# Kernel optimization log

Hardware: AMD Instinct MI355X
Metric: run time of the kernel (lower is better)

Reference implementation:

```python
import jax, jax.numpy as jnp
import numpy as np

N_NODES = 100000
N_GRAPHS = 64


def _gcn_norm(edge_index, num_nodes):
    # Add self-loops and compute symmetric normalization (PyG GCNConv gcn_norm).
    src = jnp.concatenate([edge_index[0], jnp.arange(num_nodes, dtype=edge_index.dtype)])
    dst = jnp.concatenate([edge_index[1], jnp.arange(num_nodes, dtype=edge_index.dtype)])
    deg = jax.ops.segment_sum(jnp.ones_like(dst, dtype=jnp.float32), dst, num_segments=num_nodes)
    dinv = jnp.where(deg > 0, jax.lax.rsqrt(deg), 0.0)
    norm = dinv[src] * dinv[dst]  # [E + N]
    return src, dst, norm


def _gcn_conv(x, src, dst, norm, W, b, num_nodes):
    h = x @ W                                   # [N, out]
    msg = h[src] * norm[:, None]                # gather + scale  [E+N, out]
    out = jax.ops.segment_sum(msg, dst, num_segments=num_nodes)  # scatter-add
    return out + b


def setup_inputs() -> dict:
    key = jax.random.key(0)
    ks = jax.random.split(key, 8)
    E = 1600000
    pos = jax.random.normal(ks[0], (N_NODES, 3), dtype=jnp.float32)
    edge_index = jax.random.randint(ks[1], (2, E), 0, N_NODES, dtype=jnp.int64)
    batch = jnp.sort(jax.random.randint(ks[2], (N_NODES,), 0, N_GRAPHS, dtype=jnp.int64))
    def glorot(k, shape):
        lim = np.sqrt(6.0 / (shape[0] + shape[1])).astype(np.float32)
        return jax.random.uniform(k, shape, dtype=jnp.float32, minval=-lim, maxval=lim)
    return {
        "pos": pos,
        "edge_index": edge_index,
        "batch": batch,
        "W1": glorot(ks[3], (3, 64)),  "b1": jnp.zeros((64,), jnp.float32),
        "W2": glorot(ks[4], (64, 64)), "b2": jnp.zeros((64,), jnp.float32),
        "W3": glorot(ks[5], (64, 24)), "b3": jnp.zeros((24,), jnp.float32),
    }


def reference(pos, edge_index, batch, W1, b1, W2, b2, W3, b3):
    src, dst, norm = _gcn_norm(edge_index, N_NODES)
    h = jax.nn.relu(_gcn_conv(pos, src, dst, norm, W1, b1, N_NODES))
    h = jax.nn.relu(_gcn_conv(h, src, dst, norm, W2, b2, N_NODES))
    y = _gcn_conv(h, src, dst, norm, W3, b3, N_NODES)  # [N, 24]
    # global_mean_pool over batch ids, then tanh
    sums = jax.ops.segment_sum(y, batch, num_segments=N_GRAPHS)          # [G, 24]
    counts = jax.ops.segment_sum(jnp.ones((N_NODES,), jnp.float32), batch, num_segments=N_GRAPHS)
    mean = sums / jnp.maximum(counts, 1.0)[:, None]
    return jnp.tanh(mean)
```

## Files before the change

### kernel.cpp

```cpp
#include <hip/hip_runtime.h>
#include <math.h>

#define NNODES 100000
#define NGRAPHS 64
#define NB 391
#define CAP 4608
#define NBLKA 1024
#define NBLKB 512
#define NT2 1563


__device__ __forceinline__ unsigned int f2bf(float x) {
    union { float f; unsigned int u; } v;
    v.f = x;
    unsigned int r = v.u + 0x7FFFu + ((v.u >> 16) & 1u);
    return r >> 16;
}
__device__ __forceinline__ unsigned int pack2bf(float lo, float hi) {
    return f2bf(lo) | (f2bf(hi) << 16);
}
__device__ __forceinline__ float bflo(unsigned int u) {
    union { unsigned int u; float f; } v;
    v.u = u << 16;
    return v.f;
}
__device__ __forceinline__ float bfhi(unsigned int u) {
    union { unsigned int u; float f; } v;
    v.u = u & 0xFFFF0000u;
    return v.f;
}

#define ACC8(A, ofs, V) \
    A[(ofs) + 0] += bflo((V).x); A[(ofs) + 1] += bfhi((V).x); \
    A[(ofs) + 2] += bflo((V).y); A[(ofs) + 3] += bfhi((V).y); \
    A[(ofs) + 4] += bflo((V).z); A[(ofs) + 5] += bfhi((V).z); \
    A[(ofs) + 6] += bflo((V).w); A[(ofs) + 7] += bfhi((V).w);


__device__ __forceinline__ int ntld(const int* p) { return __builtin_nontemporal_load(p); }
__device__ __forceinline__ int2 ntld2(const int2* p) {
    long long v = __builtin_nontemporal_load((const long long*)p);
    int2 r;
    r.x = (int)(unsigned int)(v & 0xffffffffLL);
    r.y = (int)(v >> 32);
    return r;
}


__global__ void bucket_scatter(const int* __restrict__ src, const int* __restrict__ dst,
                               int* __restrict__ bCur, unsigned int* __restrict__ packed,
                               int E) {
    __shared__ int h[NB];
    __shared__ int cur[NB];
    for (int k = threadIdx.x; k < NB; k += 256) h[k] = 0;
    __syncthreads();
    int base = blockIdx.x * 2048 + threadIdx.x;
    int d[8], s[8], b[8];
#pragma unroll
    for (int k = 0; k < 8; ++k) {
        int e = base + k * 256;
        if (e < E) {
            d[k] = dst[e];
            s[k] = src[e];
            b[k] = d[k] >> 8;
            atomicAdd(&h[b[k]], 1);
        }
    }
    __syncthreads();
    for (int k = threadIdx.x; k < NB; k += 256) {
        int c = h[k];
        cur[k] = c ? atomicAdd(&bCur[k], c) : 0;
    }
    __syncthreads();
#pragma unroll
    for (int k = 0; k < 8; ++k) {
        int e = base + k * 256;
        if (e < E) {
            int pos = atomicAdd(&cur[b[k]], 1);
            if (pos < CAP)
                packed[(size_t)b[k] * CAP + pos] = ((unsigned int)(d[k] & 255) << 17) | (unsigned int)s[k];
        }
    }
}

__global__ void bucket_build(const unsigned int* __restrict__ packed, const int* __restrict__ bCur,
                             const int* __restrict__ batch, const float* __restrict__ pos,
                             int2* __restrict__ rowBE, int* __restrict__ col,
                             float* __restrict__ dinv, int2* __restrict__ dg,
                             float4* __restrict__ pos4, int N_) {
    __shared__ int cnt[256];
    __shared__ int bas[256];
    int tid = threadIdx.x;
    int b = blockIdx.x;
    int count = bCur[b];
    if (count > CAP) count = CAP;
    int beg = b * CAP;
    cnt[tid] = 0;
    __syncthreads();
    for (int k = beg + tid; k < beg + count; k += 256) atomicAdd(&cnt[packed[k] >> 17], 1);
    __syncthreads();
    int myCnt = cnt[tid];
    bas[tid] = myCnt;
    __syncthreads();
    for (int off = 1; off < 256; off <<= 1) {
        int v = (tid >= off) ? bas[tid - off] : 0;
        __syncthreads();
        bas[tid] += v;
        __syncthreads();
    }
    int excl = beg + ((tid > 0) ? bas[tid - 1] : 0);
    int node = (b << 8) + tid;
    if (node < N_) {
        rowBE[node] = make_int2(excl, excl + myCnt);
        float di = rsqrtf((float)myCnt + 1.0f);
        dinv[node] = di;
        dg[node] = make_int2(__float_as_int(di), batch[node]);
        pos4[node] = make_float4(pos[node * 3] * di, pos[node * 3 + 1] * di,
                                 pos[node * 3 + 2] * di, di);
    }
    __syncthreads();
    bas[tid] = excl;
    __syncthreads();
    for (int k = beg + tid; k < beg + count; k += 256) {
        unsigned int p = packed[k];
        int pos_ = atomicAdd(&bas[p >> 17], 1);
        col[pos_] = (int)(p & 0x1FFFFu);
    }
}


__global__ void mm12_gp(const float4* __restrict__ pos4, const int2* __restrict__ rowBE,
                        const int* __restrict__ col, const float* __restrict__ dinv,
                        const float* __restrict__ W1, const float* __restrict__ b1,
                        const float* __restrict__ W2, uint2* __restrict__ outz, int n) {
    __shared__ float4 part[256];
    __shared__ float4 ag[64];
    __shared__ float xs[64][65];
    __shared__ float4 ws[64 * 16];
    const int tid = threadIdx.x;
    const int rowBase = blockIdx.x * 64;
    const int r = tid >> 2, t4 = tid & 3;
    const int i = rowBase + r;

    float sx = 0, sy = 0, sz = 0, dival = 0;
    if (i < n) {
        int2 be = rowBE[i];
        float4 ps = pos4[i];
        dival = ps.w;
        if (t4 == 0) { sx = ps.x; sy = ps.y; sz = ps.z; }
        for (int j = be.x + t4; j < be.y; j += 4) {
            float4 v = pos4[ntld(&col[j])];
            sx += v.x; sy += v.y; sz += v.z;
        }
    }
    part[tid] = make_float4(sx, sy, sz, dival);
    const float4* W24 = (const float4*)W2;
    for (int idx = tid; idx < 64 * 16; idx += 256) ws[idx] = W24[idx];
    __syncthreads();
    if (tid < 64) {
        float4 p0 = part[tid * 4], p1 = part[tid * 4 + 1];
        float4 p2 = part[tid * 4 + 2], p3 = part[tid * 4 + 3];
        ag[tid] = make_float4((p0.x + p1.x) + (p2.x + p3.x),
                              (p0.y + p1.y) + (p2.y + p3.y),
                              (p0.z + p1.z) + (p2.z + p3.z), p0.w);
    }
    __syncthreads();
    for (int idx = tid; idx < 64 * 64; idx += 256) {
        int rr = idx >> 6;
        int k = idx & 63;
        float4 a = ag[rr];
        float v = b1[k] + a.w * (a.x * W1[k] + a.y * W1[64 + k] + a.z * W1[128 + k]);
        xs[rr][k] = fmaxf(v, 0.0f);
    }
    __syncthreads();

    const int f4 = tid & 15;
    const int r0 = (tid >> 4) * 4;
    float4 a0 = make_float4(0, 0, 0, 0), a1 = a0, a2 = a0, a3 = a0;
#pragma unroll 4
    for (int k = 0; k < 64; ++k) {
        float4 wv = ws[k * 16 + f4];
        float xa = xs[r0 + 0][k];
        float xb = xs[r0 + 1][k];
        float xc = xs[r0 + 2][k];
        float xd = xs[r0 + 3][k];
        a0.x += wv.x * xa; a0.y += wv.y * xa; a0.z += wv.z * xa; a0.w += wv.w * xa;
        a1.x += wv.x * xb; a1.y += wv.y * xb; a1.z += wv.z * xb; a1.w += wv.w * xb;
        a2.x += wv.x * xc; a2.y += wv.y * xc; a2.z += wv.z * xc; a2.w += wv.w * xc;
        a3.x += wv.x * xd; a3.y += wv.y * xd; a3.z += wv.z * xd; a3.w += wv.w * xd;
    }
    int i0 = rowBase + r0;
    float d0 = (i0 + 0 < n) ? dinv[i0 + 0] : 1.0f;
    float d1 = (i0 + 1 < n) ? dinv[i0 + 1] : 1.0f;
    float d2 = (i0 + 2 < n) ? dinv[i0 + 2] : 1.0f;
    float d3 = (i0 + 3 < n) ? dinv[i0 + 3] : 1.0f;
    const size_t gsel = (size_t)(f4 >> 2) * NNODES;
    const int sub = f4 & 3;
    if (i0 + 0 < n)
        outz[(gsel + (i0 + 0)) * 4 + sub] = make_uint2(pack2bf(a0.x * d0, a0.y * d0), pack2bf(a0.z * d0, a0.w * d0));
    if (i0 + 1 < n)
        outz[(gsel + (i0 + 1)) * 4 + sub] = make_uint2(pack2bf(a1.x * d1, a1.y * d1), pack2bf(a1.z * d1, a1.w * d1));
    if (i0 + 2 < n)
        outz[(gsel + (i0 + 2)) * 4 + sub] = make_uint2(pack2bf(a2.x * d2, a2.y * d2), pack2bf(a2.z * d2, a2.w * d2));
    if (i0 + 3 < n)
        outz[(gsel + (i0 + 3)) * 4 + sub] = make_uint2(pack2bf(a3.x * d3, a3.y * d3), pack2bf(a3.z * d3, a3.w * d3));
}


__global__ void gather2_sliced(const int2* __restrict__ rowBE, const int* __restrict__ col,
                               const uint4* __restrict__ z2s, const float* __restrict__ dinv,
                               const float* __restrict__ b2, uint4* __restrict__ h2s) {
    const int tid = threadIdx.x;
    const int g = blockIdx.x / NT2;
    const int tile = blockIdx.x - g * NT2;
    const int il = tid >> 2, t4 = tid & 3;
    const int i = tile * 64 + il;
    const size_t base = (size_t)g * NNODES;

    float acc[16];
#pragma unroll
    for (int k = 0; k < 16; ++k) acc[k] = 0.0f;

    if (i < NNODES) {
        if (t4 == 0) {
            uint4 sa = z2s[(base + i) * 2 + 0];
            uint4 sb = z2s[(base + i) * 2 + 1];
            ACC8(acc, 0, sa)
            ACC8(acc, 8, sb)
        }
        int2 be = rowBE[i];
        int j = be.x + t4;
        for (; j + 4 < be.y; j += 8) {
            int s0 = ntld(&col[j]);
            int s1 = ntld(&col[j + 4]);
            uint4 a0 = z2s[(base + s0) * 2 + 0];
            uint4 b0 = z2s[(base + s0) * 2 + 1];
            uint4 a1 = z2s[(base + s1) * 2 + 0];
            uint4 b1 = z2s[(base + s1) * 2 + 1];
            ACC8(acc, 0, a0)
            ACC8(acc, 8, b0)
            ACC8(acc, 0, a1)
            ACC8(acc, 8, b1)
        }
        for (; j < be.y; j += 4) {
            int s = ntld(&col[j]);
            uint4 a = z2s[(base + s) * 2 + 0];
            uint4 b = z2s[(base + s) * 2 + 1];
            ACC8(acc, 0, a)
            ACC8(acc, 8, b)
        }
    }
#pragma unroll
    for (int k = 0; k < 16; ++k) acc[k] += __shfl_xor(acc[k], 1);
#pragma unroll
    for (int k = 0; k < 16; ++k) acc[k] += __shfl_xor(acc[k], 2);

    if (t4 == 0 && i < NNODES) {
        float di = dinv[i];
        const float* bv = b2 + g * 16;
        float h[16];
#pragma unroll
        for (int k = 0; k < 16; ++k) h[k] = fmaxf(acc[k] * di + bv[k], 0.0f);
        h2s[(base + i) * 2 + 0] = make_uint4(pack2bf(h[0], h[1]), pack2bf(h[2], h[3]),
                                             pack2bf(h[4], h[5]), pack2bf(h[6], h[7]));
        h2s[(base + i) * 2 + 1] = make_uint4(pack2bf(h[8], h[9]), pack2bf(h[10], h[11]),
                                             pack2bf(h[12], h[13]), pack2bf(h[14], h[15]));
    }
}


__device__ __forceinline__ void st_y(uint2* __restrict__ yA, uint2* __restrict__ yB,
                                     int i, int f4, uint2 v) {
    if (f4 < 4) yA[(size_t)i * 4 + f4] = v;
    else        yB[(size_t)i * 2 + (f4 - 4)] = v;
}

__global__ void mm3_b16(const uint4* __restrict__ xb, const float* __restrict__ W,
                        const float* __restrict__ dinv, uint2* __restrict__ yA,
                        uint2* __restrict__ yB, int n) {
    __shared__ float xs[128][65];
    __shared__ float4 ws[64 * 6];
    const int tid = threadIdx.x;
    const int rowBase = blockIdx.x * 128;

    for (int idx = tid; idx < 128 * 8; idx += 192) {
        int r = idx >> 3;
        int c8 = idx & 7;
        int gr = rowBase + r;
        uint4 v = (gr < n) ? xb[((size_t)(c8 >> 1) * NNODES + gr) * 2 + (c8 & 1)]
                           : make_uint4(0, 0, 0, 0);
        float* xp = &xs[r][c8 * 8];
        xp[0] = bflo(v.x); xp[1] = bfhi(v.x);
        xp[2] = bflo(v.y); xp[3] = bfhi(v.y);
        xp[4] = bflo(v.z); xp[5] = bfhi(v.z);
        xp[6] = bflo(v.w); xp[7] = bfhi(v.w);
    }
    const float4* W4 = (const float4*)W;
    for (int idx = tid; idx < 64 * 6; idx += 192) ws[idx] = W4[idx];
    __syncthreads();

    const int f4 = tid % 6;
    const int r0 = (tid / 6) * 4;
    float4 a0 = make_float4(0, 0, 0, 0), a1 = a0, a2 = a0, a3 = a0;
#pragma unroll 4
    for (int k = 0; k < 64; ++k) {
        float4 wv = ws[k * 6 + f4];
        float xa = xs[r0 + 0][k];
        float xb_ = xs[r0 + 1][k];
        float xc = xs[r0 + 2][k];
        float xd = xs[r0 + 3][k];
        a0.x += wv.x * xa; a0.y += wv.y * xa; a0.z += wv.z * xa; a0.w += wv.w * xa;
        a1.x += wv.x * xb_; a1.y += wv.y * xb_; a1.z += wv.z * xb_; a1.w += wv.w * xb_;
        a2.x += wv.x * xc; a2.y += wv.y * xc; a2.z += wv.z * xc; a2.w += wv.w * xc;
        a3.x += wv.x * xd; a3.y += wv.y * xd; a3.z += wv.z * xd; a3.w += wv.w * xd;
    }
    int i0 = rowBase + r0;
    float d0 = (i0 + 0 < n) ? dinv[i0 + 0] : 1.0f;
    float d1 = (i0 + 1 < n) ? dinv[i0 + 1] : 1.0f;
    float d2 = (i0 + 2 < n) ? dinv[i0 + 2] : 1.0f;
    float d3 = (i0 + 3 < n) ? dinv[i0 + 3] : 1.0f;
    if (i0 + 0 < n)
        st_y(yA, yB, i0 + 0, f4, make_uint2(pack2bf(a0.x * d0, a0.y * d0), pack2bf(a0.z * d0, a0.w * d0)));
    if (i0 + 1 < n)
        st_y(yA, yB, i0 + 1, f4, make_uint2(pack2bf(a1.x * d1, a1.y * d1), pack2bf(a1.z * d1, a1.w * d1)));
    if (i0 + 2 < n)
        st_y(yA, yB, i0 + 2, f4, make_uint2(pack2bf(a2.x * d2, a2.y * d2), pack2bf(a2.z * d2, a2.w * d2)));
    if (i0 + 3 < n)
        st_y(yA, yB, i0 + 3, f4, make_uint2(pack2bf(a3.x * d3, a3.y * d3), pack2bf(a3.z * d3, a3.w * d3)));
}


__global__ void gather3A(const int2* __restrict__ rowBE, const int* __restrict__ col,
                         const uint4* __restrict__ yA, const int2* __restrict__ dg,
                         float* __restrict__ partA) {
    __shared__ float lpool[NGRAPHS * 16];
    for (int k = threadIdx.x; k < NGRAPHS * 16; k += 256) lpool[k] = 0.0f;
    __syncthreads();

    const int T = NNODES * 4;
    const int stride = NBLKA * 256;
    for (int t = blockIdx.x * 256 + threadIdx.x; t < T; t += stride) {
        int i = t >> 2;
        int half = t & 1;
        int r = (t >> 1) & 1;
        int2 wi = ntld2(&dg[i]);
        float di = __int_as_float(wi.x);
        int g = wi.y;
        int2 be = ntld2(&rowBE[i]);
        int mid = be.x + ((be.y - be.x + 1) >> 1);
        int a = half ? mid : be.x;
        int b = half ? be.y : mid;
        float acc[8] = {0, 0, 0, 0, 0, 0, 0, 0};
        if (!half) {
            uint4 sv = yA[(size_t)i * 2 + r];
            acc[0] = bflo(sv.x); acc[1] = bfhi(sv.x);
            acc[2] = bflo(sv.y); acc[3] = bfhi(sv.y);
            acc[4] = bflo(sv.z); acc[5] = bfhi(sv.z);
            acc[6] = bflo(sv.w); acc[7] = bfhi(sv.w);
        }
        int j = a;
        for (; j + 8 <= b; j += 8) {
            int s[8];
            uint4 v[8];
#pragma unroll
            for (int k = 0; k < 8; ++k) s[k] = ntld(&col[j + k]);
#pragma unroll
            for (int k = 0; k < 8; ++k) v[k] = yA[(size_t)s[k] * 2 + r];
#pragma unroll
            for (int k = 0; k < 8; ++k) {
                acc[0] += bflo(v[k].x); acc[1] += bfhi(v[k].x);
                acc[2] += bflo(v[k].y); acc[3] += bfhi(v[k].y);
                acc[4] += bflo(v[k].z); acc[5] += bfhi(v[k].z);
                acc[6] += bflo(v[k].w); acc[7] += bfhi(v[k].w);
            }
        }
        for (; j < b; ++j) {
            uint4 v = yA[(size_t)ntld(&col[j]) * 2 + r];
            acc[0] += bflo(v.x); acc[1] += bfhi(v.x);
            acc[2] += bflo(v.y); acc[3] += bfhi(v.y);
            acc[4] += bflo(v.z); acc[5] += bfhi(v.z);
            acc[6] += bflo(v.w); acc[7] += bfhi(v.w);
        }
#pragma unroll
        for (int k = 0; k < 8; ++k) acc[k] += __shfl_xor(acc[k], 1);
        if (!half) {
            float* lp = &lpool[g * 16 + r * 8];
#pragma unroll
            for (int k = 0; k < 8; ++k) atomicAdd(&lp[k], acc[k] * di);
        }
    }
    __syncthreads();
    float* pp = partA + (size_t)blockIdx.x * (NGRAPHS * 16);
    for (int k = threadIdx.x; k < NGRAPHS * 16; k += 256) pp[k] = lpool[k];
}

__global__ void gather3B(const int2* __restrict__ rowBE, const int* __restrict__ col,
                         const uint4* __restrict__ yB, const int2* __restrict__ dg,
                         float* __restrict__ partB, float* __restrict__ cpart) {
    __shared__ float lpool[NGRAPHS * 8];
    __shared__ float lcnt[NGRAPHS];
    for (int k = threadIdx.x; k < NGRAPHS * 8; k += 256) lpool[k] = 0.0f;
    for (int k = threadIdx.x; k < NGRAPHS; k += 256) lcnt[k] = 0.0f;
    __syncthreads();

    const int T = NNODES * 2;
    const int stride = NBLKB * 256;
    for (int t = blockIdx.x * 256 + threadIdx.x; t < T; t += stride) {
        int i = t >> 1;
        int half = t & 1;
        int2 wi = ntld2(&dg[i]);
        float di = __int_as_float(wi.x);
        int g = wi.y;
        int2 be = ntld2(&rowBE[i]);
        int mid = be.x + ((be.y - be.x + 1) >> 1);
        int a = half ? mid : be.x;
        int b = half ? be.y : mid;
        float acc[8] = {0, 0, 0, 0, 0, 0, 0, 0};
        if (!half) {
            uint4 sv = yB[i];
            acc[0] = bflo(sv.x); acc[1] = bfhi(sv.x);
            acc[2] = bflo(sv.y); acc[3] = bfhi(sv.y);
            acc[4] = bflo(sv.z); acc[5] = bfhi(sv.z);
            acc[6] = bflo(sv.w); acc[7] = bfhi(sv.w);
        }
        int j = a;
        for (; j + 8 <= b; j += 8) {
            int s[8];
            uint4 v[8];
#pragma unroll
            for (int k = 0; k < 8; ++k) s[k] = ntld(&col[j + k]);
#pragma unroll
            for (int k = 0; k < 8; ++k) v[k] = yB[s[k]];
#pragma unroll
            for (int k = 0; k < 8; ++k) {
                acc[0] += bflo(v[k].x); acc[1] += bfhi(v[k].x);
                acc[2] += bflo(v[k].y); acc[3] += bfhi(v[k].y);
                acc[4] += bflo(v[k].z); acc[5] += bfhi(v[k].z);
                acc[6] += bflo(v[k].w); acc[7] += bfhi(v[k].w);
            }
        }
        for (; j < b; ++j) {
            uint4 v = yB[ntld(&col[j])];
            acc[0] += bflo(v.x); acc[1] += bfhi(v.x);
            acc[2] += bflo(v.y); acc[3] += bfhi(v.y);
            acc[4] += bflo(v.z); acc[5] += bfhi(v.z);
            acc[6] += bflo(v.w); acc[7] += bfhi(v.w);
        }
#pragma unroll
        for (int k = 0; k < 8; ++k) acc[k] += __shfl_xor(acc[k], 1);
        if (!half) {
            float* lp = &lpool[g * 8];
#pragma unroll
            for (int k = 0; k < 8; ++k) atomicAdd(&lp[k], acc[k] * di);
            atomicAdd(&lcnt[g], 1.0f);
        }
    }
    __syncthreads();
    float* pp = partB + (size_t)blockIdx.x * (NGRAPHS * 8);
    for (int k = threadIdx.x; k < NGRAPHS * 8; k += 256) pp[k] = lpool[k];
    float* cp = cpart + (size_t)blockIdx.x * NGRAPHS;
    for (int k = threadIdx.x; k < NGRAPHS; k += 256) cp[k] = lcnt[k];
}

__global__ void pool_finish(const float* __restrict__ partA, const float* __restrict__ partB,
                            const float* __restrict__ cpart, const float* __restrict__ b3,
                            float* __restrict__ out) {
    int w = blockIdx.x * 4 + (threadIdx.x >> 6);
    int lane = threadIdx.x & 63;
    if (w >= NGRAPHS * 24) return;
    int g = w / 24;
    int c = w - g * 24;
    float s = 0.0f, cn = 0.0f;
    if (c < 16) {
        for (int b = lane; b < NBLKA; b += 64) s += partA[(size_t)b * (NGRAPHS * 16) + g * 16 + c];
    } else {
        for (int b = lane; b < NBLKB; b += 64) s += partB[(size_t)b * (NGRAPHS * 8) + g * 8 + (c - 16)];
    }
    for (int b = lane; b < NBLKB; b += 64) cn += cpart[(size_t)b * NGRAPHS + g];
#pragma unroll
    for (int off = 32; off > 0; off >>= 1) {
        s += __shfl_down(s, off);
        cn += __shfl_down(cn, off);
    }
    if (lane == 0) out[w] = tanhf(s / fmaxf(cn, 1.0f) + b3[c]);
}


static inline int gridFor(long long total, int block) {
    return (int)((total + block - 1) / block);
}

extern "C" void kernel_launch(void* const* d_in, const int* in_sizes, int n_in,
                              void* d_out, int out_size, void* d_ws, size_t ws_size,
                              hipStream_t stream) {
    const float* pos   = (const float*)d_in[0];
    const int*   ei    = (const int*)d_in[1];
    const int*   batch = (const int*)d_in[2];
    const float* W1    = (const float*)d_in[3];
    const float* b1    = (const float*)d_in[4];
    const float* W2    = (const float*)d_in[5];
    const float* b2    = (const float*)d_in[6];
    const float* W3    = (const float*)d_in[7];
    const float* b3    = (const float*)d_in[8];
    float*       out   = (float*)d_out;

    const int N = NNODES;
    const int E = in_sizes[1] / 2;
    const int* src = ei;
    const int* dst = ei + E;

    char* p = (char*)d_ws;
    uint4*  z2s    = (uint4*)p;         p += (size_t)N * 8 * sizeof(uint4);
    uint4*  h2s    = (uint4*)p;         p += (size_t)N * 8 * sizeof(uint4);
    uint4*  yA     = (uint4*)p;         p += (size_t)N * 2 * sizeof(uint4);
    uint4*  yB     = (uint4*)p;         p += (size_t)N * 1 * sizeof(uint4);
    float4* pos4   = (float4*)p;        p += (size_t)N * sizeof(float4);
    int2*   rowBE  = (int2*)p;          p += (size_t)N * sizeof(int2);
    int2*   dg     = (int2*)p;          p += (size_t)N * sizeof(int2);
    float*  dinv   = (float*)p;         p += (size_t)N * sizeof(float);
    int*    bCur   = (int*)p;           p += NB * sizeof(int);
    unsigned int* packed = (unsigned int*)p;  p += (size_t)NB * CAP * sizeof(unsigned int);
    int*    col    = (int*)p;           p += (size_t)NB * CAP * sizeof(int);
    float*  partA  = (float*)z2s;
    float*  partB  = partA + (size_t)NBLKA * NGRAPHS * 16;
    float*  cpartB = partB + (size_t)NBLKB * NGRAPHS * 8;

    const int B = 256;
    const int edgeBlocks = gridFor(E, 2048);

    hipMemsetAsync(bCur, 0, NB * sizeof(int), stream);
    bucket_scatter<<<edgeBlocks, 256, 0, stream>>>(src, dst, bCur, packed, E);
    bucket_build<<<NB, 256, 0, stream>>>(packed, bCur, batch, pos, rowBE, col, dinv, dg, pos4, N);

    mm12_gp<<<gridFor(N, 64), 256, 0, stream>>>(pos4, rowBE, col, dinv, W1, b1, W2, (uint2*)z2s, N);

    gather2_sliced<<<4 * NT2, 256, 0, stream>>>(rowBE, col, z2s, dinv, b2, h2s);

    mm3_b16<<<gridFor(N, 128), 192, 0, stream>>>(h2s, W3, dinv, (uint2*)yA, (uint2*)yB, N);

    gather3A<<<NBLKA, 256, 0, stream>>>(rowBE, col, yA, dg, partA);
    gather3B<<<NBLKB, 256, 0, stream>>>(rowBE, col, yB, dg, partB, cpartB);
    pool_finish<<<gridFor((long long)NGRAPHS * 24 * 64, B), B, 0, stream>>>(partA, partB, cpartB, b3, out);
}
```

Baseline: 287.6 us.

## Split gather2 into per-slice launches with two threads per node

The layer-2 aggregation kernel now assigns two threads per node, each owning half of a 16-feature slice, instead of four threads striding the edge list and reducing with shuffles. The four feature slices are launched as four separate kernels rather than one grid indexed by slice. This removes the cross-lane shuffle reduction and gives each thread longer sequential edge loops with four independent gathers in flight. In exchange it adds three extra launches, and per-thread edge work grows for high-degree nodes.

```diff
diff --git a/kernel.cpp b/kernel.cpp
--- a/kernel.cpp
+++ b/kernel.cpp
@@ -7,7 +7,6 @@
 #define CAP 4608
 #define NBLKA 1024
 #define NBLKB 512
-#define NT2 1563
 
 
 __device__ __forceinline__ unsigned int f2bf(float x) {
@@ -209,63 +208,49 @@
 
 __global__ void gather2_sliced(const int2* __restrict__ rowBE, const int* __restrict__ col,
                                const uint4* __restrict__ z2s, const float* __restrict__ dinv,
-                               const float* __restrict__ b2, uint4* __restrict__ h2s) {
+                               const float* __restrict__ b2, uint4* __restrict__ h2s, int g) {
     const int tid = threadIdx.x;
-    const int g = blockIdx.x / NT2;
-    const int tile = blockIdx.x - g * NT2;
-    const int il = tid >> 2, t4 = tid & 3;
-    const int i = tile * 64 + il;
+    const int il = tid >> 1, t2 = tid & 1;
+    const int i = blockIdx.x * 128 + il;
+    if (i >= NNODES) return;
     const size_t base = (size_t)g * NNODES;
 
-    float acc[16];
-#pragma unroll
-    for (int k = 0; k < 16; ++k) acc[k] = 0.0f;
-
-    if (i < NNODES) {
-        if (t4 == 0) {
-            uint4 sa = z2s[(base + i) * 2 + 0];
-            uint4 sb = z2s[(base + i) * 2 + 1];
-            ACC8(acc, 0, sa)
-            ACC8(acc, 8, sb)
-        }
-        int2 be = rowBE[i];
-        int j = be.x + t4;
-        for (; j + 4 < be.y; j += 8) {
-            int s0 = ntld(&col[j]);
-            int s1 = ntld(&col[j + 4]);
-            uint4 a0 = z2s[(base + s0) * 2 + 0];
-            uint4 b0 = z2s[(base + s0) * 2 + 1];
-            uint4 a1 = z2s[(base + s1) * 2 + 0];
-            uint4 b1 = z2s[(base + s1) * 2 + 1];
-            ACC8(acc, 0, a0)
-            ACC8(acc, 8, b0)
-            ACC8(acc, 0, a1)
-            ACC8(acc, 8, b1)
-        }
-        for (; j < be.y; j += 4) {
-            int s = ntld(&col[j]);
-            uint4 a = z2s[(base + s) * 2 + 0];
-            uint4 b = z2s[(base + s) * 2 + 1];
-            ACC8(acc, 0, a)
-            ACC8(acc, 8, b)
-        }
-    }
-#pragma unroll
-    for (int k = 0; k < 16; ++k) acc[k] += __shfl_xor(acc[k], 1);
-#pragma unroll
-    for (int k = 0; k < 16; ++k) acc[k] += __shfl_xor(acc[k], 2);
-
-    if (t4 == 0 && i < NNODES) {
-        float di = dinv[i];
-        const float* bv = b2 + g * 16;
-        float h[16];
-#pragma unroll
-        for (int k = 0; k < 16; ++k) h[k] = fmaxf(acc[k] * di + bv[k], 0.0f);
-        h2s[(base + i) * 2 + 0] = make_uint4(pack2bf(h[0], h[1]), pack2bf(h[2], h[3]),
-                                             pack2bf(h[4], h[5]), pack2bf(h[6], h[7]));
-        h2s[(base + i) * 2 + 1] = make_uint4(pack2bf(h[8], h[9]), pack2bf(h[10], h[11]),
-                                             pack2bf(h[12], h[13]), pack2bf(h[14], h[15]));
-    }
+    float acc[8];
+    {
+        uint4 sv = z2s[(base + i) * 2 + t2];
+        acc[0] = bflo(sv.x); acc[1] = bfhi(sv.x);
+        acc[2] = bflo(sv.y); acc[3] = bfhi(sv.y);
+        acc[4] = bflo(sv.z); acc[5] = bfhi(sv.z);
+        acc[6] = bflo(sv.w); acc[7] = bfhi(sv.w);
+    }
+    const int2 be = rowBE[i];
+    int j = be.x;
+    for (; j + 4 <= be.y; j += 4) {
+        int s0 = ntld(&col[j + 0]);
+        int s1 = ntld(&col[j + 1]);
+        int s2 = ntld(&col[j + 2]);
+        int s3 = ntld(&col[j + 3]);
+        uint4 v0 = z2s[(base + s0) * 2 + t2];
+        uint4 v1 = z2s[(base + s1) * 2 + t2];
+        uint4 v2 = z2s[(base + s2) * 2 + t2];
+        uint4 v3 = z2s[(base + s3) * 2 + t2];
+        ACC8(acc, 0, v0)
+        ACC8(acc, 0, v1)
+        ACC8(acc, 0, v2)
+        ACC8(acc, 0, v3)
+    }
+    for (; j < be.y; ++j) {
+        uint4 v = z2s[(base + (size_t)ntld(&col[j])) * 2 + t2];
+        ACC8(acc, 0, v)
+    }
+
+    const float di = dinv[i];
+    const float* bv = b2 + g * 16 + t2 * 8;
+    float h[8];
+#pragma unroll
+    for (int k = 0; k < 8; ++k) h[k] = fmaxf(acc[k] * di + bv[k], 0.0f);
+    h2s[(base + i) * 2 + t2] = make_uint4(pack2bf(h[0], h[1]), pack2bf(h[2], h[3]),
+                                          pack2bf(h[4], h[5]), pack2bf(h[6], h[7]));
 }
 
 
@@ -534,7 +519,8 @@
 
     mm12_gp<<<gridFor(N, 64), 256, 0, stream>>>(pos4, rowBE, col, dinv, W1, b1, W2, (uint2*)z2s, N);
 
-    gather2_sliced<<<4 * NT2, 256, 0, stream>>>(rowBE, col, z2s, dinv, b2, h2s);
+    for (int g = 0; g < 4; ++g)
+        gather2_sliced<<<gridFor((long long)N * 2, B), B, 0, stream>>>(rowBE, col, z2s, dinv, b2, h2s, g);
 
     mm3_b16<<<gridFor(N, 128), 192, 0, stream>>>(h2s, W3, dinv, (uint2*)yA, (uint2*)yB, N);
 
```

Result: slower. 304.3 us (+5.8%).
